# Optimization experiments

Hardware: AMD Instinct MI355X
Metric: run time of the kernel (lower is better)

The kernel has to match this reference:

```python
import jax, jax.numpy as jnp
from jax import lax
import numpy as np

B, C, H, W = 8, 64, 56, 56
LM = 9              # level_map: NSCT subbands per channel
D = LM * C + C      # 640: swin block dim
DEPTH = 2
WIN = 7
HEADS = 8
KS = 5              # NSCT filter kernel size


def _nsct_filters():
    # fixed nonsubsampled 9-band filter bank (lowpass + 8 directional), stand-in for myNSCTd
    r = np.arange(KS) - KS // 2
    yy, xx = np.meshgrid(r, r, indexing='ij')
    g = np.exp(-(xx ** 2 + yy ** 2) / 4.0)
    g = g / g.sum()
    f = [g]
    for k in range(LM - 1):
        th = k * np.pi / (LM - 1)
        d = (np.cos(th) * xx + np.sin(th) * yy) * g
        d = d - d.mean()
        d = d / np.sqrt((d ** 2).sum())
        f.append(d)
    return jnp.asarray(np.stack(f), dtype=jnp.float32)  # [LM,KS,KS]


def _ct(x):
    # per-(b,c) NSCT decomposition -> [B, LM*C, H, W], band-major (matches transpose(0,2,1,3,4).reshape)
    Bx, Cx, Hx, Wx = x.shape
    K = _nsct_filters()
    k = jnp.tile(K, (Cx, 1, 1))[:, None]  # [Cx*LM,1,KS,KS], out channel index c*LM+band
    o = lax.conv_general_dilated(x, k, (1, 1), 'SAME',
                                 dimension_numbers=('NCHW', 'OIHW', 'NCHW'),
                                 feature_group_count=Cx)
    o = o.reshape(Bx, Cx, LM, Hx, Wx).transpose(0, 2, 1, 3, 4).reshape(Bx, LM * Cx, Hx, Wx)
    return o


def _ict(y):
    # inverse transform: reshape(B,LM,C,H,W).permute(0,2,1,3,4), reconstruct per channel
    Bx = y.shape[0]
    t = y.reshape(Bx, LM, C, H, W).transpose(0, 2, 1, 3, 4).reshape(Bx, C * LM, H, W)
    K = _nsct_filters()
    g = jnp.broadcast_to(K, (C, LM, KS, KS))  # groups=C: 9 subbands -> 1 channel each
    return lax.conv_general_dilated(t, g, (1, 1), 'SAME',
                                    dimension_numbers=('NCHW', 'OIHW', 'NCHW'),
                                    feature_group_count=C)


def _ln(x, g, b):
    m = x.mean(-1, keepdims=True)
    v = x.var(-1, keepdims=True)
    return (x - m) / jnp.sqrt(v + 1e-5) * g + b


def _attn_mask(shift):
    # standard SW-MSA mask for shifted windows
    img = np.zeros((H, W), np.int32)
    c = 0
    for hs in (slice(0, -WIN), slice(-WIN, -shift), slice(-shift, None)):
        for ws in (slice(0, -WIN), slice(-WIN, -shift), slice(-shift, None)):
            img[hs, ws] = c
            c += 1
    a = img.reshape(H // WIN, WIN, W // WIN, WIN).transpose(0, 2, 1, 3).reshape(-1, WIN * WIN)
    m = np.where(a[:, :, None] != a[:, None, :], -1e9, 0.0).astype(np.float32)
    return jnp.asarray(m)  # [nWindows, T, T]


def _swin_block(x, p, shift):
    Bx = x.shape[0]
    T = WIN * WIN
    dh = D // HEADS
    nH, nWw = H // WIN, W // WIN
    sc = x
    h = _ln(x, p['ln1_g'], p['ln1_b'])
    if shift:
        h = jnp.roll(h, (-shift, -shift), (1, 2))
    w = h.reshape(Bx, nH, WIN, nWw, WIN, D).transpose(0, 1, 3, 2, 4, 5).reshape(Bx * nH * nWw, T, D)
    qkv = w @ p['qkv_w'] + p['qkv_b']
    q, k, v = jnp.split(qkv, 3, axis=-1)
    heads = lambda t: t.reshape(-1, T, HEADS, dh).transpose(0, 2, 1, 3)
    q, k, v = heads(q), heads(k), heads(v)
    s = jnp.einsum('nhtd,nhsd->nhts', q, k) / jnp.sqrt(jnp.asarray(dh, x.dtype))
    if shift:
        m = _attn_mask(shift)
        s = (s.reshape(Bx, nH * nWw, HEADS, T, T) + m[None, :, None]).reshape(-1, HEADS, T, T)
    a = jax.nn.softmax(s, -1)
    o = jnp.einsum('nhts,nhsd->nhtd', a, v).transpose(0, 2, 1, 3).reshape(-1, T, D)
    o = o @ p['proj_w'] + p['proj_b']
    o = o.reshape(Bx, nH, nWw, WIN, WIN, D).transpose(0, 1, 3, 2, 4, 5).reshape(Bx, H, W, D)
    if shift:
        o = jnp.roll(o, (shift, shift), (1, 2))
    x = sc + o
    h2 = _ln(x, p['ln2_g'], p['ln2_b'])
    h2 = jax.nn.gelu(h2 @ p['fc1_w'] + p['fc1_b']) @ p['fc2_w'] + p['fc2_b']
    return x + h2


def setup_inputs() -> dict:
    key = jax.random.key(0)
    ks = jax.random.split(key, 8)
    s = 0.02
    n = lambda k, shp: jax.random.normal(k, shp, jnp.float32) * s
    return {
        'x': jax.random.normal(ks[0], (B, C, H, W), jnp.float32),
        'ln1_g': jnp.ones((DEPTH, D), jnp.float32), 'ln1_b': jnp.zeros((DEPTH, D), jnp.float32),
        'qkv_w': n(ks[1], (DEPTH, D, 3 * D)), 'qkv_b': jnp.zeros((DEPTH, 3 * D), jnp.float32),
        'proj_w': n(ks[2], (DEPTH, D, D)), 'proj_b': jnp.zeros((DEPTH, D), jnp.float32),
        'ln2_g': jnp.ones((DEPTH, D), jnp.float32), 'ln2_b': jnp.zeros((DEPTH, D), jnp.float32),
        'fc1_w': n(ks[3], (DEPTH, D, 4 * D)), 'fc1_b': jnp.zeros((DEPTH, 4 * D), jnp.float32),
        'fc2_w': n(ks[4], (DEPTH, 4 * D, D)), 'fc2_b': jnp.zeros((DEPTH, D), jnp.float32),
        'lin_w': n(ks[5], (D, LM * C)), 'lin_b': jnp.zeros((LM * C,), jnp.float32),
        'conv_w': n(ks[6], (C, D)), 'conv_b': jnp.zeros((C,), jnp.float32),
    }


def reference(x, ln1_g, ln1_b, qkv_w, qkv_b, proj_w, proj_b, ln2_g, ln2_b,
              fc1_w, fc1_b, fc2_w, fc2_b, lin_w, lin_b, conv_w, conv_b):
    x2 = jax.nn.relu(x)
    x_trans = lax.stop_gradient(_ct(x2))          # CT detaches its input in the original
    x3 = jnp.concatenate([x_trans, x2], axis=1)   # [B, 10C, H, W]
    x3 = x3.transpose(0, 2, 3, 1)                 # BHWC
    for i in range(DEPTH):
        p = dict(ln1_g=ln1_g[i], ln1_b=ln1_b[i], qkv_w=qkv_w[i], qkv_b=qkv_b[i],
                 proj_w=proj_w[i], proj_b=proj_b[i], ln2_g=ln2_g[i], ln2_b=ln2_b[i],
                 fc1_w=fc1_w[i], fc1_b=fc1_b[i], fc2_w=fc2_w[i], fc2_b=fc2_b[i])
        x3 = _swin_block(x3, p, 0 if i % 2 == 0 else WIN // 2)
    x3 = x3 @ lin_w + lin_b                        # D -> LM*C
    y = x3.transpose(0, 3, 1, 2)                   # [B, 9C, H, W]
    y_trans = lax.stop_gradient(_ict(y))           # ICT detaches its input in the original
    yc = jnp.concatenate([y_trans, y], axis=1)     # [B, 10C, H, W]
    out = jnp.einsum('bchw,oc->bohw', yc, conv_w) + conv_b[None, :, None, None]
    return out
```

## Files before the change

### kernel.cpp

```cpp
#include <hip/hip_runtime.h>
#include <hip/hip_bf16.h>
#include <math.h>

typedef __attribute__((ext_vector_type(4))) float f32x4;
typedef __attribute__((ext_vector_type(8))) short short8;

#define NTOK 25088
#define DD   640

__device__ __forceinline__ void gload_lds16(const void* g, void* l) {
    __builtin_amdgcn_global_load_lds((const __attribute__((address_space(1))) void*)g,
                                     (__attribute__((address_space(3))) void*)l,
                                     16, 0, 0);
}

__device__ __forceinline__ float gelu_f(float t) {
    float u = 1.5957691216057308f * (t + 0.044715f * t * t * t);
    float e = __builtin_amdgcn_exp2f(u * -1.4426950408889634f);
    return t / (1.f + e);
}

__global__ void init_consts(float* __restrict__ filt, float* __restrict__ linbp,
                            const float* __restrict__ lin_b, float* __restrict__ convbp,
                            const float* __restrict__ conv_b) {
    int t = threadIdx.x;
    if (t == 0) {
        float g[25]; float s = 0.f;
        for (int i = 0; i < 5; i++) for (int j = 0; j < 5; j++) {
            float yy = (float)(i - 2), xx = (float)(j - 2);
            float v = expf(-(xx*xx + yy*yy) * 0.25f);
            g[i*5+j] = v; s += v;
        }
        for (int i = 0; i < 25; i++) { g[i] /= s; filt[i] = g[i]; }
        for (int k = 0; k < 8; k++) {
            float th = (float)k * 3.14159265358979323846f / 8.f;
            float ct = cosf(th), st = sinf(th);
            float d[25]; float mean = 0.f;
            for (int i = 0; i < 5; i++) for (int j = 0; j < 5; j++) {
                float yy = (float)(i - 2), xx = (float)(j - 2);
                d[i*5+j] = (ct*xx + st*yy) * g[i*5+j];
                mean += d[i*5+j];
            }
            mean *= (1.f/25.f);
            float ss = 0.f;
            for (int i = 0; i < 25; i++) { d[i] -= mean; ss += d[i]*d[i]; }
            ss = sqrtf(ss);
            for (int i = 0; i < 25; i++) filt[(k+1)*25 + i] = d[i] / ss;
        }
    }
    for (int i = t; i < 640; i += 256) linbp[i]  = (i < 576) ? lin_b[i]  : 0.f;
    for (int i = t; i < 128; i += 256) convbp[i] = (i < 64)  ? conv_b[i] : 0.f;
}

__global__ __launch_bounds__(256)
void wtrans_kernel(const float* __restrict__ src, __hip_bfloat16* __restrict__ dst,
                   int K, int Nsrc) {
    __shared__ float tile[32][33];
    const int n0 = blockIdx.x * 32;
    const int k0 = blockIdx.y * 32;
    const int tx = threadIdx.x, ty = threadIdx.y;
    #pragma unroll
    for (int r = ty; r < 32; r += 8) {
        int k = k0 + r, n = n0 + tx;
        tile[r][tx] = (n < Nsrc) ? src[(long)k * Nsrc + n] : 0.f;
    }
    __syncthreads();
    #pragma unroll
    for (int r = ty; r < 32; r += 8) {
        int n = n0 + r, k = k0 + tx;
        dst[(long)n * K + k] = __float2bfloat16(tile[tx][r]);
    }
}

__global__ void wcast_kernel(const float* __restrict__ src, __hip_bfloat16* __restrict__ dst,
                             int count, int total) {
    int i = blockIdx.x * 256 + threadIdx.x;
    if (i < total) dst[i] = __float2bfloat16(i < count ? src[i] : 0.f);
}

__global__ __launch_bounds__(256)
void prep_kernel(const float* __restrict__ x, const float* __restrict__ filt,
                 float* __restrict__ x3) {
    __shared__ float sf[225];
    for (int i = threadIdx.x; i < 225; i += 256) sf[i] = filt[i];
    __syncthreads();
    int id = blockIdx.x * 256 + threadIdx.x;
    int c = id & 63;
    int pix = id >> 6;
    int w = pix % 56, h = (pix / 56) % 56, b = pix / 3136;
    const float* xp = x + (long)(b * 64 + c) * 3136;
    float nb[25];
    #pragma unroll
    for (int dy = 0; dy < 5; dy++) {
        int hy = h + dy - 2;
        #pragma unroll
        for (int dx = 0; dx < 5; dx++) {
            int wx = w + dx - 2;
            float v = 0.f;
            if (hy >= 0 && hy < 56 && wx >= 0 && wx < 56) v = fmaxf(xp[hy*56 + wx], 0.f);
            nb[dy*5 + dx] = v;
        }
    }
    float* orow = x3 + (long)pix * DD;
    #pragma unroll
    for (int band = 0; band < 9; band++) {
        float a = 0.f;
        #pragma unroll
        for (int t = 0; t < 25; t++) a += nb[t] * sf[band*25 + t];
        orow[band*64 + c] = a;
    }
    orow[576 + c] = nb[12];
}

__global__ __launch_bounds__(256)
void ln_kernel(const float* __restrict__ xin, const float* __restrict__ g,
               const float* __restrict__ bt, __hip_bfloat16* __restrict__ out) {
    const int lane = threadIdx.x & 63;
    const long tok = (long)blockIdx.x * 4 + (threadIdx.x >> 6);
    const float* xr = xin + tok * DD;
    float v[10]; float s = 0.f, s2 = 0.f;
    #pragma unroll
    for (int i = 0; i < 10; i++) { float t = xr[lane + (i << 6)]; v[i] = t; s += t; s2 += t*t; }
    #pragma unroll
    for (int o = 32; o > 0; o >>= 1) { s += __shfl_down(s, o); s2 += __shfl_down(s2, o); }
    s = __shfl(s, 0); s2 = __shfl(s2, 0);
    const float mean = s * (1.f/640.f);
    const float var  = s2 * (1.f/640.f) - mean * mean;
    const float inv  = 1.f / sqrtf(var + 1e-5f);
    __hip_bfloat16* orow = out + tok * DD;
    #pragma unroll
    for (int i = 0; i < 10; i++) {
        int c = lane + (i << 6);
        orow[c] = __float2bfloat16((v[i] - mean) * inv * g[c] + bt[c]);
    }
}

__global__ __launch_bounds__(256, 2)
void gemm128_kernel(const __hip_bfloat16* __restrict__ A,
                    const __hip_bfloat16* __restrict__ Bt,
                    const float* __restrict__ bias,
                    const float* __restrict__ resid,
                    float* __restrict__ Cf,
                    __hip_bfloat16* __restrict__ Cb,
                    int K, int ldc, int ncf, int ldb, int col_off, int ncb,
                    int act_gelu, int nvalid, int mode) {
    extern __shared__ __align__(16) char smraw[];
    __hip_bfloat16* sm = (__hip_bfloat16*)smraw;

    const int tid  = threadIdx.x;
    const int lane = tid & 63;
    const int wv   = tid >> 6;
    const int wr   = wv >> 1;
    const int wc   = wv & 1;

    const int gx   = gridDim.x;
    const int nwg  = gx * gridDim.y;
    const int orig = blockIdx.y * gx + blockIdx.x;
    const int qq = nwg >> 3, rr = nwg & 7;
    const int xcd = orig & 7, lid = orig >> 3;
    const int wg = (xcd < rr ? xcd * (qq + 1) : rr * (qq + 1) + (xcd - rr) * qq) + lid;
    const long m0 = (long)(wg / gx) * 128;
    const long n0 = (long)(wg % gx) * 128;

    const bool wact = ((int)n0 + (wc << 6)) < nvalid;

    f32x4 acc[4][4];
    #pragma unroll
    for (int i = 0; i < 4; i++)
        #pragma unroll
        for (int j = 0; j < 4; j++) acc[i][j] = (f32x4){0.f, 0.f, 0.f, 0.f};

    const int srow  = tid >> 3;
    const int slot  = tid & 7;
    const int sslot = slot ^ (srow & 7);
    const __hip_bfloat16* Agb = A  + (m0 + srow) * (long)K + (sslot << 3);
    const __hip_bfloat16* Bgb = Bt + (n0 + srow) * (long)K + (sslot << 3);
    __hip_bfloat16* dA = sm + srow * 64 + (slot << 3);
    __hip_bfloat16* dB = sm + 8192 + srow * 64 + (slot << 3);

    const int frow = lane & 15;
    const int fks  = lane >> 4;
    const int fr7  = frow & 7;

    auto STAGE = [&](int b, int k0) {
        #pragma unroll
        for (int i = 0; i < 4; i++) {
            gload_lds16(Agb + (long)i * 32 * K + k0, dA + b * 16384 + i * 2048);
            gload_lds16(Bgb + (long)i * 32 * K + k0, dB + b * 16384 + i * 2048);
        }
    };

#define COMPUTE(BUFOFF)                                                                     \
    do {                                                                                    \
        const __hip_bfloat16* pA = sm + (BUFOFF);                                           \
        const __hip_bfloat16* pB = sm + 8192 + (BUFOFF);                                    \
        if (wact) {                                                                         \
            _Pragma("unroll")                                                               \
            for (int ks = 0; ks < 2; ++ks) {                                                \
                short8 af[4], bfr[4];                                                       \
                _Pragma("unroll")                                                           \
                for (int mi = 0; mi < 4; ++mi) {                                            \
                    const int R = (wr << 6) + (mi << 4) + frow;                             \
                    af[mi] = *(const short8*)(pA + R * 64 +                                 \
                              ((((ks << 2) | fks) ^ (R & 7)) << 3));                        \
                }                                                                           \
                _Pragma("unroll")                                                           \
                for (int nj = 0; nj < 4; ++nj) {                                            \
                    const int Rn = (wc << 6) + (nj << 4) + frow;                            \
                    bfr[nj] = *(const short8*)(pB + Rn * 64 +                               \
                               ((((ks << 2) | fks) ^ (Rn & 7)) << 3));                      \
                }                                                                           \
                __builtin_amdgcn_s_setprio(1);                                              \
                _Pragma("unroll")                                                           \
                for (int mi = 0; mi < 4; ++mi)                                              \
                    _Pragma("unroll")                                                       \
                    for (int nj = 0; nj < 4; ++nj)     \
                        acc[mi][nj] = __builtin_amdgcn_mfma_f32_16x16x32_bf16(              \
                            bfr[nj], af[mi], acc[mi][nj], 0, 0, 0);                         \
                __builtin_amdgcn_s_setprio(0);                                              \
            }                                                                               \
        }                                                                                   \
    } while (0)

    const int nt = K >> 6;
    STAGE(0, 0);
    for (int t2 = 0; t2 < nt; t2 += 2) {
        if (t2 + 1 < nt) {
            STAGE(1, (t2 + 1) << 6);
            asm volatile("s_waitcnt vmcnt(8)" ::: "memory");
        } else {
            asm volatile("s_waitcnt vmcnt(0)" ::: "memory");
        }
        __builtin_amdgcn_s_barrier();
        __builtin_amdgcn_sched_barrier(0);
        COMPUTE(0);
        asm volatile("" ::: "memory");
        __builtin_amdgcn_s_barrier();
        if (t2 + 2 < nt) {
            STAGE(0, (t2 + 2) << 6);
            asm volatile("s_waitcnt vmcnt(8)" ::: "memory");
        } else {
            asm volatile("s_waitcnt vmcnt(0)" ::: "memory");
        }
        __builtin_amdgcn_s_barrier();
        __builtin_amdgcn_sched_barrier(0);
        COMPUTE(16384);
        asm volatile("" ::: "memory");
        __builtin_amdgcn_s_barrier();
    }
#undef COMPUTE

    if (!wact) return;
    const int nlim = (ncf > ncb) ? ncf : ncb;
    #pragma unroll
    for (int mi = 0; mi < 4; ++mi) {
        const long row = m0 + (wr << 6) + (mi << 4) + frow;
        #pragma unroll
        for (int nj = 0; nj < 4; ++nj) {
            const int n = (int)n0 + (wc << 6) + (nj << 4) + (fks << 2);
            if (n >= nlim) continue;
            f32x4 v = acc[mi][nj];
            if (bias) {
                const f32x4 bv = *(const f32x4*)&bias[n];
                v += bv;
            }
            if (act_gelu) {
                v[0] = gelu_f(v[0]); v[1] = gelu_f(v[1]); v[2] = gelu_f(v[2]); v[3] = gelu_f(v[3]);
            }
            if (mode == 1) {
                const int b = (int)(row / 3136), pos = (int)(row % 3136);
                #pragma unroll
                for (int r = 0; r < 4; ++r)
                    Cf[(long)(b * 64 + n + r) * 3136 + pos] = v[r];
                continue;
            }
            if (resid && n < ncf) v += *(const f32x4*)&resid[row * (long)ldc + n];
            if (Cf && n < ncf) *(f32x4*)&Cf[row * (long)ldc + n] = v;
            if (Cb && n < ncb) {
                short4 p;
                p.x = (short)__bfloat16_as_short(__float2bfloat16(v[0]));
                p.y = (short)__bfloat16_as_short(__float2bfloat16(v[1]));
                p.z = (short)__bfloat16_as_short(__float2bfloat16(v[2]));
                p.w = (short)__bfloat16_as_short(__float2bfloat16(v[3]));
                *(short4*)&Cb[row * (long)ldb + col_off + n] = p;
            }
        }
    }
}

__global__ __launch_bounds__(256)
void attn_kernel(const __hip_bfloat16* __restrict__ qkv, __hip_bfloat16* __restrict__ o,
                 int shift) {
    __shared__ __align__(16) float qT[80][52];
    __shared__ __align__(16) float kT[80][52];
    __shared__ __align__(16) float vs[50][80];
    __shared__ __align__(16) float ss[49][52];
    __shared__ int toks[49];
    __shared__ int rid[49];

    const int tid = threadIdx.x;
    const int win = blockIdx.x >> 3;
    const int hd  = blockIdx.x & 7;
    const int b   = win >> 6;
    const int wh  = (win >> 3) & 7;
    const int ww  = win & 7;

    if (tid < 49) {
        int i = tid / 7, j = tid % 7;
        int ph = wh * 7 + i, pw = ww * 7 + j;
        int sh = ph + shift; if (sh >= 56) sh -= 56;
        int sw = pw + shift; if (sw >= 56) sw -= 56;
        toks[tid] = (b * 56 + sh) * 56 + sw;
        int rh = (ph < 49) ? 0 : ((ph < 53) ? 1 : 2);
        int rw = (pw < 49) ? 0 : ((pw < 53) ? 1 : 2);
        rid[tid] = rh * 3 + rw;
    }
    for (int i = tid; i < 80 * 3; i += 256) {
        int d = i / 3, cc = 49 + (i % 3);
        qT[d][cc] = 0.f; kT[d][cc] = 0.f;
    }
    __syncthreads();
    for (int idx = tid; idx < 49 * 80; idx += 256) {
        int t = idx / 80, d = idx % 80;
        long base = (long)toks[t] * 1920 + hd * 80 + d;
        qT[d][t] = __bfloat162float(qkv[base]);
        kT[d][t] = __bfloat162float(qkv[base + 640]);
        vs[t][d] = __bfloat162float(qkv[base + 1280]);
    }
    __syncthreads();
    const float scale = 0.11180339887498948f;
    for (int p = tid; p < 49 * 13; p += 256) {
        int t = p / 13, j0 = (p % 13) * 4;
        float4 a = {0.f, 0.f, 0.f, 0.f};
        #pragma unroll
        for (int d = 0; d < 80; d++) {
            float qv = qT[d][t];
            float4 kv = *(const float4*)&kT[d][j0];
            a.x += qv * kv.x; a.y += qv * kv.y; a.z += qv * kv.z; a.w += qv * kv.w;
        }
        a.x *= scale; a.y *= scale; a.z *= scale; a.w *= scale;
        *(float4*)&ss[t][j0] = a;
    }
    __syncthreads();
    if (tid < 196) {
        const int r = tid >> 2, sub = tid & 3;
        const int j0 = sub * 13;
        const int j1 = (sub == 3) ? 10 : 13;
        const int myr = rid[r];
        float mx = -1e30f;
        for (int i = 0; i < j1; i++) {
            float v = ss[r][j0 + i];
            if (shift && rid[j0 + i] != myr) v = -1e9f;
            ss[r][j0 + i] = v;
            mx = fmaxf(mx, v);
        }
        mx = fmaxf(mx, __shfl_xor(mx, 1));
        mx = fmaxf(mx, __shfl_xor(mx, 2));
        float sum = 0.f;
        for (int i = 0; i < j1; i++) {
            float e = __expf(ss[r][j0 + i] - mx);
            ss[r][j0 + i] = e;
            sum += e;
        }
        sum += __shfl_xor(sum, 1);
        sum += __shfl_xor(sum, 2);
        const float inv = 1.f / sum;
        for (int i = 0; i < j1; i++) ss[r][j0 + i] *= inv;
    }
    __syncthreads();
    for (int p = tid; p < 49 * 20; p += 256) {
        int t = p / 20, dv = (p % 20) * 4;
        float4 a = {0.f, 0.f, 0.f, 0.f};
        for (int j = 0; j < 49; j++) {
            float w = ss[t][j];
            float4 vv = *(const float4*)&vs[j][dv];
            a.x += w * vv.x; a.y += w * vv.y; a.z += w * vv.z; a.w += w * vv.w;
        }
        long base = (long)toks[t] * DD + hd * 80 + dv;
        o[base + 0] = __float2bfloat16(a.x);
        o[base + 1] = __float2bfloat16(a.y);
        o[base + 2] = __float2bfloat16(a.z);
        o[base + 3] = __float2bfloat16(a.w);
    }
}

__global__ __launch_bounds__(256)
void ict_kernel(const float* __restrict__ y, const float* __restrict__ filt,
                __hip_bfloat16* __restrict__ ayc) {
    __shared__ float sf[225];
    for (int i = threadIdx.x; i < 225; i += 256) sf[i] = filt[i];
    __syncthreads();
    int id = blockIdx.x * 256 + threadIdx.x;
    int c4 = (id & 15) << 2;
    int pix = id >> 4;
    int w = pix % 56, h = (pix / 56) % 56, b = pix / 3136;
    float4 a = {0.f, 0.f, 0.f, 0.f};
    #pragma unroll
    for (int dy = 0; dy < 5; dy++) {
        int hy = h + dy - 2;
        if (hy < 0 || hy >= 56) continue;
        #pragma unroll
        for (int dx = 0; dx < 5; dx++) {
            int wx = w + dx - 2;
            if (wx < 0 || wx >= 56) continue;
            const float* yr = y + ((long)(b * 56 + hy) * 56 + wx) * DD + c4;
            #pragma unroll
            for (int band = 0; band < 9; band++) {
                const float f = sf[band*25 + dy*5 + dx];
                const float4 vv = *(const float4*)&yr[band * 64];
                a.x += vv.x * f; a.y += vv.y * f; a.z += vv.z * f; a.w += vv.w * f;
            }
        }
    }
    short4 p;
    p.x = (short)__bfloat16_as_short(__float2bfloat16(a.x));
    p.y = (short)__bfloat16_as_short(__float2bfloat16(a.y));
    p.z = (short)__bfloat16_as_short(__float2bfloat16(a.z));
    p.w = (short)__bfloat16_as_short(__float2bfloat16(a.w));
    *(short4*)&ayc[(long)pix * DD + c4] = p;
}

extern "C" void kernel_launch(void* const* d_in, const int* in_sizes, int n_in,
                              void* d_out, int out_size, void* d_ws, size_t ws_size,
                              hipStream_t stream) {
    (void)in_sizes; (void)n_in; (void)out_size; (void)ws_size;
    const float* x      = (const float*)d_in[0];
    const float* ln1_g  = (const float*)d_in[1];
    const float* ln1_b  = (const float*)d_in[2];
    const float* qkv_w  = (const float*)d_in[3];
    const float* qkv_b  = (const float*)d_in[4];
    const float* proj_w = (const float*)d_in[5];
    const float* proj_b = (const float*)d_in[6];
    const float* ln2_g  = (const float*)d_in[7];
    const float* ln2_b  = (const float*)d_in[8];
    const float* fc1_w  = (const float*)d_in[9];
    const float* fc1_b  = (const float*)d_in[10];
    const float* fc2_w  = (const float*)d_in[11];
    const float* fc2_b  = (const float*)d_in[12];
    const float* lin_w  = (const float*)d_in[13];
    const float* lin_b  = (const float*)d_in[14];
    const float* conv_w = (const float*)d_in[15];
    const float* conv_b = (const float*)d_in[16];

    char* ws = (char*)d_ws;
    size_t off = 0;
    auto alloc = [&](size_t bytes) -> void* {
        void* p = ws + off;
        off += (bytes + 255) & ~(size_t)255;
        return p;
    };
    float* filt   = (float*)alloc(225 * 4);
    float* linbp  = (float*)alloc(640 * 4);
    float* convbp = (float*)alloc(128 * 4);
    __hip_bfloat16* qkvWt[2], *projWt[2], *fc1Wt[2], *fc2Wt[2];
    for (int i = 0; i < 2; i++) qkvWt[i] = (__hip_bfloat16*)alloc(1920L * 640 * 2);
    for (int i = 0; i < 2; i++) projWt[i] = (__hip_bfloat16*)alloc(640L * 640 * 2);
    for (int i = 0; i < 2; i++) fc1Wt[i] = (__hip_bfloat16*)alloc(2560L * 640 * 2);
    for (int i = 0; i < 2; i++) fc2Wt[i] = (__hip_bfloat16*)alloc(640L * 2560 * 2);
    __hip_bfloat16* linWt  = (__hip_bfloat16*)alloc(640L * 640 * 2);
    __hip_bfloat16* convWt = (__hip_bfloat16*)alloc(128L * 640 * 2);
    float* x3 = (float*)alloc((long)NTOK * DD * 4);
    __hip_bfloat16* bufA = (__hip_bfloat16*)alloc((long)NTOK * DD * 2);
    char* bufB = (char*)alloc((long)NTOK * 2560 * 2);
    __hip_bfloat16* qkv = (__hip_bfloat16*)bufB;
    __hip_bfloat16* h2  = (__hip_bfloat16*)bufB;
    float* ybuf = (float*)bufB;
    __hip_bfloat16* ayc = (__hip_bfloat16*)(bufB + (long)NTOK * DD * 4);

    hipFuncSetAttribute((const void*)gemm128_kernel,
                        hipFuncAttributeMaxDynamicSharedMemorySize, 65536);

    dim3 tb(32, 8);
    init_consts<<<1, 256, 0, stream>>>(filt, linbp, lin_b, convbp, conv_b);
    for (int i = 0; i < 2; i++) {
        wtrans_kernel<<<dim3(60, 20), tb, 0, stream>>>(qkv_w + (long)i*640*1920, qkvWt[i], 640, 1920);
        wtrans_kernel<<<dim3(20, 20), tb, 0, stream>>>(proj_w + (long)i*640*640,  projWt[i], 640, 640);
        wtrans_kernel<<<dim3(80, 20), tb, 0, stream>>>(fc1_w + (long)i*640*2560, fc1Wt[i], 640, 2560);
        wtrans_kernel<<<dim3(20, 80), tb, 0, stream>>>(fc2_w + (long)i*2560*640, fc2Wt[i], 2560, 640);
    }
    wtrans_kernel<<<dim3(20, 20), tb, 0, stream>>>(lin_w, linWt, 640, 576);
    wcast_kernel<<<320, 256, 0, stream>>>(conv_w, convWt, 64 * 640, 128 * 640);

    prep_kernel<<<6272, 256, 0, stream>>>(x, filt, x3);

    for (int i = 0; i < 2; i++) {
        int shift = i ? 3 : 0;
        ln_kernel<<<6272, 256, 0, stream>>>(x3, ln1_g + i*640, ln1_b + i*640, bufA);
        gemm128_kernel<<<dim3(15, 196), 256, 65536, stream>>>(bufA, qkvWt[i], qkv_b + i*1920,
            nullptr, nullptr, qkv, 640, 0, 0, 1920, 0, 1920, 0, 1920, 0);
        attn_kernel<<<4096, 256, 0, stream>>>(qkv, bufA, shift);
        gemm128_kernel<<<dim3(5, 196), 256, 65536, stream>>>(bufA, projWt[i], proj_b + i*640,
            x3, x3, nullptr, 640, 640, 640, 0, 0, 0, 0, 640, 0);
        ln_kernel<<<6272, 256, 0, stream>>>(x3, ln2_g + i*640, ln2_b + i*640, bufA);
        gemm128_kernel<<<dim3(20, 196), 256, 65536, stream>>>(bufA, fc1Wt[i], fc1_b + i*2560,
            nullptr, nullptr, h2, 640, 0, 0, 2560, 0, 2560, 1, 2560, 0);
        gemm128_kernel<<<dim3(5, 196), 256, 65536, stream>>>(h2, fc2Wt[i], fc2_b + i*640,
            x3, x3, (i == 1) ? bufA : nullptr, 2560, 640, 640, 640, 0, (i == 1) ? 640 : 0, 0, 640, 0);
    }
    gemm128_kernel<<<dim3(5, 196), 256, 65536, stream>>>(bufA, linWt, linbp,
        nullptr, ybuf, ayc, 640, 640, 640, 640, 64, 576, 0, 576, 0);
    ict_kernel<<<1568, 256, 0, stream>>>(ybuf, filt, ayc);
    gemm128_kernel<<<dim3(1, 196), 256, 65536, stream>>>(ayc, convWt, convbp,
        nullptr, (float*)d_out, nullptr, 640, 0, 64, 0, 0, 0, 0, 64, 1);
}
```

Baseline: 1.442 ms.

## Switch GEMM to 4-stage BK=32 LDS pipeline with single barrier per step

```diff
diff --git a/kernel.cpp b/kernel.cpp
--- a/kernel.cpp
+++ b/kernel.cpp
@@ -145,7 +145,6 @@
                     int K, int ldc, int ncf, int ldb, int col_off, int ncb,
                     int act_gelu, int nvalid, int mode) {
     extern __shared__ __align__(16) char smraw[];
-    __hip_bfloat16* sm = (__hip_bfloat16*)smraw;
 
     const int tid  = threadIdx.x;
     const int lane = tid & 63;
@@ -170,85 +169,55 @@
         #pragma unroll
         for (int j = 0; j < 4; j++) acc[i][j] = (f32x4){0.f, 0.f, 0.f, 0.f};
 
-    const int srow  = tid >> 3;
-    const int slot  = tid & 7;
-    const int sslot = slot ^ (srow & 7);
-    const __hip_bfloat16* Agb = A  + (m0 + srow) * (long)K + (sslot << 3);
-    const __hip_bfloat16* Bgb = Bt + (n0 + srow) * (long)K + (sslot << 3);
-    __hip_bfloat16* dA = sm + srow * 64 + (slot << 3);
-    __hip_bfloat16* dB = sm + 8192 + srow * 64 + (slot << 3);
+    const int r0  = tid >> 2;
+    const int sl  = tid & 3;
+    const int ssl = sl ^ ((r0 >> 1) & 3);
+    const __hip_bfloat16* Agb = A  + (m0 + r0) * (long)K + (ssl << 3);
+    const __hip_bfloat16* Bgb = Bt + (n0 + r0) * (long)K + (ssl << 3);
+    char* dA = smraw + r0 * 64 + sl * 16;
+    char* dB = dA + 8192;
 
     const int frow = lane & 15;
     const int fks  = lane >> 4;
-    const int fr7  = frow & 7;
-
-    auto STAGE = [&](int b, int k0) {
-        #pragma unroll
-        for (int i = 0; i < 4; i++) {
-            gload_lds16(Agb + (long)i * 32 * K + k0, dA + b * 16384 + i * 2048);
-            gload_lds16(Bgb + (long)i * 32 * K + k0, dB + b * 16384 + i * 2048);
-        }
+    const int colA = (fks ^ ((frow >> 1) & 3)) << 4;
+
+    auto STAGE = [&](int b, int kt) {
+        const long ko = (long)kt << 5;
+        gload_lds16(Agb + ko,             dA + b * 16384);
+        gload_lds16(Agb + 64 * (long)K + ko, dA + b * 16384 + 4096);
+        gload_lds16(Bgb + ko,             dB + b * 16384);
+        gload_lds16(Bgb + 64 * (long)K + ko, dB + b * 16384 + 4096);
     };
 
-#define COMPUTE(BUFOFF)                                                                     \
-    do {                                                                                    \
-        const __hip_bfloat16* pA = sm + (BUFOFF);                                           \
-        const __hip_bfloat16* pB = sm + 8192 + (BUFOFF);                                    \
-        if (wact) {                                                                         \
-            _Pragma("unroll")                                                               \
-            for (int ks = 0; ks < 2; ++ks) {                                                \
-                short8 af[4], bfr[4];                                                       \
-                _Pragma("unroll")                                                           \
-                for (int mi = 0; mi < 4; ++mi) {                                            \
-                    const int R = (wr << 6) + (mi << 4) + frow;                             \
-                    af[mi] = *(const short8*)(pA + R * 64 +                                 \
-                              ((((ks << 2) | fks) ^ (R & 7)) << 3));                        \
-                }                                                                           \
-                _Pragma("unroll")                                                           \
-                for (int nj = 0; nj < 4; ++nj) {                                            \
-                    const int Rn = (wc << 6) + (nj << 4) + frow;                            \
-                    bfr[nj] = *(const short8*)(pB + Rn * 64 +                               \
-                               ((((ks << 2) | fks) ^ (Rn & 7)) << 3));                      \
-                }                                                                           \
-                __builtin_amdgcn_s_setprio(1);                                              \
-                _Pragma("unroll")                                                           \
-                for (int mi = 0; mi < 4; ++mi)                                              \
-                    _Pragma("unroll")                                                       \
-                    for (int nj = 0; nj < 4; ++nj)     \
-                        acc[mi][nj] = __builtin_amdgcn_mfma_f32_16x16x32_bf16(              \
-                            bfr[nj], af[mi], acc[mi][nj], 0, 0, 0);                         \
-                __builtin_amdgcn_s_setprio(0);                                              \
-            }                                                                               \
-        }                                                                                   \
-    } while (0)
-
-    const int nt = K >> 6;
-    STAGE(0, 0);
-    for (int t2 = 0; t2 < nt; t2 += 2) {
-        if (t2 + 1 < nt) {
-            STAGE(1, (t2 + 1) << 6);
-            asm volatile("s_waitcnt vmcnt(8)" ::: "memory");
-        } else {
-            asm volatile("s_waitcnt vmcnt(0)" ::: "memory");
-        }
+    const int nt = K >> 5;
+    STAGE(0, 0); STAGE(1, 1); STAGE(2, 2);
+    for (int t = 0; t < nt; ++t) {
+        if (t + 3 < nt)      asm volatile("s_waitcnt vmcnt(8)" ::: "memory");
+        else if (t + 2 < nt) asm volatile("s_waitcnt vmcnt(4)" ::: "memory");
+        else                 asm volatile("s_waitcnt vmcnt(0)" ::: "memory");
         __builtin_amdgcn_s_barrier();
         __builtin_amdgcn_sched_barrier(0);
-        COMPUTE(0);
-        asm volatile("" ::: "memory");
-        __builtin_amdgcn_s_barrier();
-        if (t2 + 2 < nt) {
-            STAGE(0, (t2 + 2) << 6);
-            asm volatile("s_waitcnt vmcnt(8)" ::: "memory");
-        } else {
-            asm volatile("s_waitcnt vmcnt(0)" ::: "memory");
-        }
-        __builtin_amdgcn_s_barrier();
-        __builtin_amdgcn_sched_barrier(0);
-        COMPUTE(16384);
-        asm volatile("" ::: "memory");
-        __builtin_amdgcn_s_barrier();
-    }
-#undef COMPUTE
+        if (t + 3 < nt) STAGE((t + 3) & 3, t + 3);
+        if (wact) {
+            const char* pA = smraw + (t & 3) * 16384;
+            const char* pB = pA + 8192;
+            short8 af[4], bfr[4];
+            #pragma unroll
+            for (int mi = 0; mi < 4; ++mi)
+                af[mi] = *(const short8*)(pA + ((wr << 6) + (mi << 4) + frow) * 64 + colA);
+            #pragma unroll
+            for (int nj = 0; nj < 4; ++nj)
+                bfr[nj] = *(const short8*)(pB + ((wc << 6) + (nj << 4) + frow) * 64 + colA);
+            __builtin_amdgcn_s_setprio(1);
+            #pragma unroll
+            for (int mi = 0; mi < 4; ++mi)
+                #pragma unroll
+                for (int nj = 0; nj < 4; ++nj)
+                    acc[mi][nj] = __builtin_amdgcn_mfma_f32_16x16x32_bf16(
+                        bfr[nj], af[mi], acc[mi][nj], 0, 0, 0);
+            __builtin_amdgcn_s_setprio(0);
+        }
+    }
 
     if (!wact) return;
     const int nlim = (ncf > ncb) ? ncf : ncb;
```

Measured after the change: 1.478 ms. +2.5%, slower.
